# Optimization experiments

Measured on AMD Instinct MI355X. Metric: run time of the kernel, lower is better.

Reference implementation:

```python
import jax, jax.numpy as jnp
import numpy as np

B, S, D, H = 32, 512, 512, 1024  # batch, seq, latents_dims, hidden (=prod(out_dims))


def setup_inputs() -> dict:
    key = jax.random.key(0)
    ks = jax.random.split(key, 7)
    scale_ih = 1.0 / np.sqrt(D)
    scale_hh = 1.0 / np.sqrt(H)
    return {
        "x": jax.random.normal(ks[0], (B, S, D), dtype=jnp.float32),
        "h0": jax.random.uniform(ks[1], (B, H), dtype=jnp.float32),
        "c0": jax.random.uniform(ks[2], (B, H), dtype=jnp.float32),
        "W_ih": jax.random.normal(ks[3], (4 * H, D), dtype=jnp.float32) * scale_ih,
        "W_hh": jax.random.normal(ks[4], (4 * H, H), dtype=jnp.float32) * scale_hh,
        "b_ih": jax.random.normal(ks[5], (4 * H,), dtype=jnp.float32) * scale_hh,
        "b_hh": jax.random.normal(ks[6], (4 * H,), dtype=jnp.float32) * scale_hh,
    }


def reference(x, h0, c0, W_ih, W_hh, b_ih, b_hh):
    # Single-layer LSTM, PyTorch gate order (i, f, g, o).
    # Precompute the input projection for all timesteps in one GEMM: [B,S,4H]
    x_proj = jnp.einsum("bsd,gd->bsg", x, W_ih) + b_ih + b_hh
    xs = jnp.swapaxes(x_proj, 0, 1)  # [S, B, 4H]

    def step(carry, xp_t):
        h, c = carry  # [B, H] each
        gates = xp_t + h @ W_hh.T  # [B, 4H]
        i, f, g, o = jnp.split(gates, 4, axis=-1)
        i = jax.nn.sigmoid(i)
        f = jax.nn.sigmoid(f)
        g = jnp.tanh(g)
        o = jax.nn.sigmoid(o)
        c = f * c + i * g
        h = o * jnp.tanh(c)
        return (h, c), h

    _, hs = jax.lax.scan(step, (h0, c0), xs)  # hs: [S, B, H]
    out = jnp.swapaxes(hs, 0, 1)  # [B, S, H]
    # view(*x.shape[:2], *out_dims) with out_dims=[1024] is a no-op reshape
    return out.reshape(B, S, H)
```

## Files before the change

kernel.cpp:

```cpp
#include <hip/hip_runtime.h>

typedef __bf16 bf16_t;
typedef __bf16 bf16x8 __attribute__((ext_vector_type(8)));
typedef __bf16 bf16x4 __attribute__((ext_vector_type(4)));
typedef __bf16 bf16x2 __attribute__((ext_vector_type(2)));
typedef float f32x16 __attribute__((ext_vector_type(16)));
typedef int i32x4 __attribute__((ext_vector_type(4)));

#define SZ_XBF    (16384ull*512*2)
#define SZ_WIH    (4096ull*512*2)
#define SZ_WHH    (4096ull*1024*2)
#define SZ_XPROJ  (16384ull*4096*2)
#define SZ_HTR    (513ull*32*1024*2)
#define OFF_XBF   (0ull)
#define OFF_WIH   (OFF_XBF + SZ_XBF)
#define OFF_WHH   (OFF_WIH + SZ_WIH)
#define OFF_XPROJ (OFF_WHH + SZ_WHH)
#define OFF_HTR   (OFF_XPROJ + SZ_XPROJ)


__global__ __launch_bounds__(256) void convert_pack(
    const float* __restrict__ x, const float* __restrict__ h0,
    const float* __restrict__ Wih, const float* __restrict__ Whh,
    bf16_t* __restrict__ xbf, bf16_t* __restrict__ wihbf,
    bf16_t* __restrict__ whhbf, bf16_t* __restrict__ htr)
{
  long long v = (long long)blockIdx.x * 256 + threadIdx.x;
  if (v < 2097152LL) {
    long long fi = v * 4;
    int b = (int)(fi >> 18);
    int rem = (int)(fi & 0x3FFFF);
    int s = rem >> 9, d = rem & 511;
    float4 f = *(const float4*)(x + fi);
    bf16x4 o; o.x = (bf16_t)f.x; o.y = (bf16_t)f.y; o.z = (bf16_t)f.z; o.w = (bf16_t)f.w;
    *(bf16x4*)(xbf + ((long long)(s*32 + b)*512 + d)) = o;
  } else if (v < 2621440LL) {
    long long fi = (v - 2097152LL) * 4;
    float4 f = *(const float4*)(Wih + fi);
    bf16x4 o; o.x = (bf16_t)f.x; o.y = (bf16_t)f.y; o.z = (bf16_t)f.z; o.w = (bf16_t)f.w;
    *(bf16x4*)(wihbf + fi) = o;
  } else if (v < 3670016LL) {
    long long fi = (v - 2621440LL) * 4;
    float4 f = *(const float4*)(Whh + fi);
    bf16x4 o; o.x = (bf16_t)f.x; o.y = (bf16_t)f.y; o.z = (bf16_t)f.z; o.w = (bf16_t)f.w;
    *(bf16x4*)(whhbf + fi) = o;
  } else if (v < 3678208LL) {
    long long fi = (v - 3670016LL) * 4;
    int b = (int)(fi >> 10), c = (int)(fi & 1023);
    float4 f = *(const float4*)(h0 + fi);
    bf16x4 o; o.x = (bf16_t)f.x; o.y = (bf16_t)f.y; o.z = (bf16_t)f.z; o.w = (bf16_t)f.w;
    *(bf16x4*)(htr + (long long)(c >> 4) * 512 + b * 16 + (c & 15)) = o;
  } else if (v < 5775360LL) {
    long long idx = v - 3678208LL;
    *(int4*)(htr + 32768LL + idx * 8) = make_int4(-1, -1, -1, -1);
  }
}

__global__ __launch_bounds__(256) void xproj_gemm(
    const bf16_t* __restrict__ Xb, const bf16_t* __restrict__ Wb,
    const float* __restrict__ bih, const float* __restrict__ bhh,
    bf16_t* __restrict__ XP)
{
  __shared__ bf16_t As[128*64];
  __shared__ bf16_t Bs[128*64];
  const int tid = threadIdx.x;
  const int lane = tid & 63, wave = tid >> 6;
  const int mhalf = wave & 1, nhalf = wave >> 1;
  const int l31 = lane & 31, khi = lane >> 5;
  const int m0 = blockIdx.x * 128, n0 = blockIdx.y * 128;

  f32x16 acc[2][2] = {};

  for (int kb = 0; kb < 8; ++kb) {
    const int k0 = kb * 64;
    __syncthreads();
#pragma unroll
    for (int j = 0; j < 4; ++j) {
      int cid = j * 256 + tid;
      int r = cid >> 3, bs = cid & 7;
      int bb = bs ^ (r & 7);
      *(bf16x8*)(As + cid * 8) = *(const bf16x8*)(Xb + (long long)(m0 + r) * 512 + k0 + bb * 8);
      *(bf16x8*)(Bs + cid * 8) = *(const bf16x8*)(Wb + (long long)(n0 + r) * 512 + k0 + bb * 8);
    }
    __syncthreads();
#pragma unroll
    for (int ks = 0; ks < 4; ++ks) {
      int blk = ks * 2 + khi;
      bf16x8 af[2], bfr[2];
#pragma unroll
      for (int mt = 0; mt < 2; ++mt) {
        int r = mhalf * 64 + mt * 32 + l31;
        af[mt] = *(const bf16x8*)(As + (r * 8 + (blk ^ (r & 7))) * 8);
      }
#pragma unroll
      for (int nt = 0; nt < 2; ++nt) {
        int r = nhalf * 64 + nt * 32 + l31;
        bfr[nt] = *(const bf16x8*)(Bs + (r * 8 + (blk ^ (r & 7))) * 8);
      }
#pragma unroll
      for (int mt = 0; mt < 2; ++mt)
#pragma unroll
        for (int nt = 0; nt < 2; ++nt)
          acc[mt][nt] = __builtin_amdgcn_mfma_f32_32x32x16_bf16(af[mt], bfr[nt], acc[mt][nt], 0, 0, 0);
    }
  }
#pragma unroll
  for (int nt = 0; nt < 2; ++nt) {
    int ng = n0 + nhalf * 64 + nt * 32 + l31;
    float bias = bih[ng] + bhh[ng];
#pragma unroll
    for (int mt = 0; mt < 2; ++mt) {
#pragma unroll
      for (int r = 0; r < 16; ++r) {
        int row = (r & 3) + 8 * (r >> 2) + 4 * khi;
        long long mg = m0 + mhalf * 64 + mt * 32 + row;
        XP[mg * 4096 + ng] = (bf16_t)(acc[mt][nt][r] + bias);
      }
    }
  }
}

__device__ __forceinline__ float sigf(float x) { return 1.0f / (1.0f + __expf(-x)); }
__device__ __forceinline__ float tanhfast(float x) {
  float e = __expf(-2.0f * fabsf(x));
  float t = (1.0f - e) / (1.0f + e);
  return copysignf(t, x);
}
__device__ __forceinline__ unsigned umax2(unsigned a, unsigned b) { return a > b ? a : b; }
__device__ __forceinline__ unsigned umax4(i32x4 v) {
  return umax2(umax2((unsigned)v[0], (unsigned)v[1]),
               umax2((unsigned)v[2], (unsigned)v[3]));
}

#define LD16(dst, ptr, OFF) \
  asm volatile("global_load_dwordx4 %0, %1, off offset:" OFF " sc0 sc1" \
               : "=v"(dst) : "v"(ptr) : "memory")

__global__ __launch_bounds__(256, 1) void lstm_rec(
    const bf16_t* __restrict__ Whh_b, const bf16_t* __restrict__ XP,
    const float* __restrict__ c0, float* __restrict__ OUT,
    bf16_t* __restrict__ HTR)
{
  const int tid = threadIdx.x;
  const int lane = tid & 63, wave = tid >> 6;
  const int ntile = wave & 1, khalf = wave >> 1;
  const int wg = blockIdx.x;
  const int l31 = lane & 31, khi = lane >> 5;

  const int nl = ntile * 32 + l31;
  const int grow = (nl >> 4) * 1024 + wg * 16 + (nl & 15);
  const int kbase = khalf * 512 + khi * 8;
  bf16x8 wreg[32];
#pragma unroll
  for (int s = 0; s < 32; ++s)
    wreg[s] = *(const bf16x8*)(Whh_b + (long long)grow * 1024 + kbase + s * 16);

  const char* abase = (const char*)HTR + khalf * 32768 + l31 * 32 + khi * 16;

  __shared__ float gLb[2][2][32][65];
  const int m_e = tid >> 3;
  const int jp = (tid & 7) * 2;
  float cr0 = c0[m_e * 1024 + wg * 16 + jp];
  float cr1 = c0[m_e * 1024 + wg * 16 + jp + 1];

  float xp[4][2];
  {
    const bf16_t* xpb = XP + (long long)m_e * 4096 + wg * 16 + jp;
#pragma unroll
    for (int g = 0; g < 4; ++g) {
      bf16x2 v = *(const bf16x2*)(xpb + g * 1024);
      xp[g][0] = (float)v.x; xp[g][1] = (float)v.y;
    }
  }

  float po0 = 0.0f, po1 = 0.0f;

  for (int t = 0; t < 512; ++t) {
    const char* p0 = abase + ((long long)t << 16);
    const char* p1 = p0 + 4096;  const char* p2 = p0 + 8192;
    const char* p3 = p0 + 12288; const char* p4 = p0 + 16384;
    const char* p5 = p0 + 20480; const char* p6 = p0 + 24576;
    const char* p7 = p0 + 28672;
    i32x4 a[32];
    for (;;) {
      LD16(a[0],  p0, "0"); LD16(a[1],  p0, "1024"); LD16(a[2],  p0, "2048"); LD16(a[3],  p0, "3072");
      LD16(a[4],  p1, "0"); LD16(a[5],  p1, "1024"); LD16(a[6],  p1, "2048"); LD16(a[7],  p1, "3072");
      LD16(a[8],  p2, "0"); LD16(a[9],  p2, "1024"); LD16(a[10], p2, "2048"); LD16(a[11], p2, "3072");
      LD16(a[12], p3, "0"); LD16(a[13], p3, "1024"); LD16(a[14], p3, "2048"); LD16(a[15], p3, "3072");
      LD16(a[16], p4, "0"); LD16(a[17], p4, "1024"); LD16(a[18], p4, "2048"); LD16(a[19], p4, "3072");
      LD16(a[20], p5, "0"); LD16(a[21], p5, "1024"); LD16(a[22], p5, "2048"); LD16(a[23], p5, "3072");
      LD16(a[24], p6, "0"); LD16(a[25], p6, "1024"); LD16(a[26], p6, "2048"); LD16(a[27], p6, "3072");
      LD16(a[28], p7, "0"); LD16(a[29], p7, "1024"); LD16(a[30], p7, "2048"); LD16(a[31], p7, "3072");
      asm volatile("s_waitcnt vmcnt(0)" ::: "memory");
      __builtin_amdgcn_sched_barrier(0);
      unsigned mA = 0, mB = 0, mC = 0, mD = 0;
#pragma unroll
      for (int s = 0; s < 32; s += 4) {
        mA = umax2(mA, umax4(a[s]));
        mB = umax2(mB, umax4(a[s + 1]));
        mC = umax2(mC, umax4(a[s + 2]));
        mD = umax2(mD, umax4(a[s + 3]));
      }
      unsigned mx = umax2(umax2(mA, mB), umax2(mC, mD));
      if (!__any((int)(mx == 0xFFFFFFFFu))) break;
    }

    if (t > 0)
      *(float2*)(OUT + ((long long)m_e * 512 + (t - 1)) * 1024 + wg * 16 + jp) =
          make_float2(po0, po1);

    f32x16 acc0 = {}, acc1 = {};
#pragma unroll
    for (int s = 0; s < 16; ++s)
      acc0 = __builtin_amdgcn_mfma_f32_32x32x16_bf16(
          __builtin_bit_cast(bf16x8, a[s]), wreg[s], acc0, 0, 0, 0);
#pragma unroll
    for (int s = 16; s < 32; ++s)
      acc1 = __builtin_amdgcn_mfma_f32_32x32x16_bf16(
          __builtin_bit_cast(bf16x8, a[s]), wreg[s], acc1, 0, 0, 0);

    float (*gp)[32][65] = gLb[t & 1];
#pragma unroll
    for (int r = 0; r < 16; ++r) {
      int mm = (r & 3) + 8 * (r >> 2) + 4 * khi;
      gp[khalf][mm][nl] = acc0[r] + acc1[r];
    }
    __syncthreads();

    float hv[2];
    {
      float ir  = gp[0][m_e][jp]      + gp[1][m_e][jp]      + xp[0][0];
      float fr  = gp[0][m_e][16 + jp] + gp[1][m_e][16 + jp] + xp[1][0];
      float gr  = gp[0][m_e][32 + jp] + gp[1][m_e][32 + jp] + xp[2][0];
      float orr = gp[0][m_e][48 + jp] + gp[1][m_e][48 + jp] + xp[3][0];
      float c = sigf(fr) * cr0 + sigf(ir) * tanhfast(gr);
      cr0 = c;
      hv[0] = sigf(orr) * tanhfast(c);
    }
    {
      int j = jp + 1;
      float ir  = gp[0][m_e][j]      + gp[1][m_e][j]      + xp[0][1];
      float fr  = gp[0][m_e][16 + j] + gp[1][m_e][16 + j] + xp[1][1];
      float gr  = gp[0][m_e][32 + j] + gp[1][m_e][32 + j] + xp[2][1];
      float orr = gp[0][m_e][48 + j] + gp[1][m_e][48 + j] + xp[3][1];
      float c = sigf(fr) * cr1 + sigf(ir) * tanhfast(gr);
      cr1 = c;
      hv[1] = sigf(orr) * tanhfast(c);
    }

    {
      bf16x2 h2; h2.x = (bf16_t)hv[0]; h2.y = (bf16_t)hv[1];
      unsigned int u = __builtin_bit_cast(unsigned int, h2);
      unsigned int* dst = (unsigned int*)(HTR + (long long)(t + 1) * 32768 +
                                          (long long)wg * 512 + m_e * 16 + jp);
      __hip_atomic_store(dst, u, __ATOMIC_RELAXED, __HIP_MEMORY_SCOPE_AGENT);
    }
    po0 = hv[0]; po1 = hv[1];

    if (t < 511) {
      const bf16_t* xpb = XP + ((long long)(t + 1) * 32 + m_e) * 4096 + wg * 16 + jp;
#pragma unroll
      for (int g = 0; g < 4; ++g) {
        bf16x2 v = *(const bf16x2*)(xpb + g * 1024);
        xp[g][0] = (float)v.x; xp[g][1] = (float)v.y;
      }
    }
  }
  *(float2*)(OUT + ((long long)m_e * 512 + 511) * 1024 + wg * 16 + jp) =
      make_float2(po0, po1);
}

extern "C" void kernel_launch(void* const* d_in, const int* in_sizes, int n_in,
                              void* d_out, int out_size, void* d_ws, size_t ws_size,
                              hipStream_t stream)
{
  const float* x   = (const float*)d_in[0];
  const float* h0  = (const float*)d_in[1];
  const float* c0  = (const float*)d_in[2];
  const float* Wih = (const float*)d_in[3];
  const float* Whh = (const float*)d_in[4];
  const float* bih = (const float*)d_in[5];
  const float* bhh = (const float*)d_in[6];
  float* out = (float*)d_out;

  char* ws = (char*)d_ws;
  bf16_t* xbf   = (bf16_t*)(ws + OFF_XBF);
  bf16_t* wihbf = (bf16_t*)(ws + OFF_WIH);
  bf16_t* whhbf = (bf16_t*)(ws + OFF_WHH);
  bf16_t* xproj = (bf16_t*)(ws + OFF_XPROJ);
  bf16_t* htr   = (bf16_t*)(ws + OFF_HTR);

  convert_pack<<<22560, 256, 0, stream>>>(x, h0, Wih, Whh, xbf, wihbf, whhbf, htr);
  xproj_gemm<<<dim3(128, 32), 256, 0, stream>>>(xbf, wihbf, bih, bhh, xproj);
  lstm_rec<<<64, 256, 0, stream>>>(whhbf, xproj, c0, out, htr);
}
```

Baseline: 1.786 ms.

## Split recurrent GEMM K across four waves, each covering both N tiles

Each of the four waves now owns a quarter of the K dimension and computes both 32-column gate tiles, instead of splitting into two N tiles times two K halves. Each wave loads half as much h data per step (16 instead of 32 vectors) and reuses each A fragment for two MFMAs. The spin-wait poll covers less data, which may shorten the critical path. The cost is a larger shared buffer and four partial sums to add in the gate epilogue instead of two.

```diff
diff --git a/kernel.cpp b/kernel.cpp
--- a/kernel.cpp
+++ b/kernel.cpp
@@ -143,21 +143,23 @@
 {
   const int tid = threadIdx.x;
   const int lane = tid & 63, wave = tid >> 6;
-  const int ntile = wave & 1, khalf = wave >> 1;
+  const int kq = wave;
   const int wg = blockIdx.x;
   const int l31 = lane & 31, khi = lane >> 5;
 
-  const int nl = ntile * 32 + l31;
-  const int grow = (nl >> 4) * 1024 + wg * 16 + (nl & 15);
-  const int kbase = khalf * 512 + khi * 8;
-  bf16x8 wreg[32];
-#pragma unroll
-  for (int s = 0; s < 32; ++s)
-    wreg[s] = *(const bf16x8*)(Whh_b + (long long)grow * 1024 + kbase + s * 16);
-
-  const char* abase = (const char*)HTR + khalf * 32768 + l31 * 32 + khi * 16;
-
-  __shared__ float gLb[2][2][32][65];
+  const int g0row = (l31 >> 4) * 1024 + wg * 16 + (l31 & 15);
+  const int g1row = (2 + (l31 >> 4)) * 1024 + wg * 16 + (l31 & 15);
+  const int kqb = kq * 256 + khi * 8;
+  bf16x8 w0[16], w1[16];
+#pragma unroll
+  for (int s = 0; s < 16; ++s) {
+    w0[s] = *(const bf16x8*)(Whh_b + (long long)g0row * 1024 + kqb + s * 16);
+    w1[s] = *(const bf16x8*)(Whh_b + (long long)g1row * 1024 + kqb + s * 16);
+  }
+
+  const char* abase = (const char*)HTR + kq * 16384 + l31 * 32 + khi * 16;
+
+  __shared__ float gLb[2][4][32][65];
   const int m_e = tid >> 3;
   const int jp = (tid & 7) * 2;
   float cr0 = c0[m_e * 1024 + wg * 16 + jp];
@@ -177,25 +179,20 @@
 
   for (int t = 0; t < 512; ++t) {
     const char* p0 = abase + ((long long)t << 16);
-    const char* p1 = p0 + 4096;  const char* p2 = p0 + 8192;
-    const char* p3 = p0 + 12288; const char* p4 = p0 + 16384;
-    const char* p5 = p0 + 20480; const char* p6 = p0 + 24576;
-    const char* p7 = p0 + 28672;
-    i32x4 a[32];
+    const char* p1 = p0 + 4096;
+    const char* p2 = p0 + 8192;
+    const char* p3 = p0 + 12288;
+    i32x4 a[16];
     for (;;) {
       LD16(a[0],  p0, "0"); LD16(a[1],  p0, "1024"); LD16(a[2],  p0, "2048"); LD16(a[3],  p0, "3072");
       LD16(a[4],  p1, "0"); LD16(a[5],  p1, "1024"); LD16(a[6],  p1, "2048"); LD16(a[7],  p1, "3072");
       LD16(a[8],  p2, "0"); LD16(a[9],  p2, "1024"); LD16(a[10], p2, "2048"); LD16(a[11], p2, "3072");
       LD16(a[12], p3, "0"); LD16(a[13], p3, "1024"); LD16(a[14], p3, "2048"); LD16(a[15], p3, "3072");
-      LD16(a[16], p4, "0"); LD16(a[17], p4, "1024"); LD16(a[18], p4, "2048"); LD16(a[19], p4, "3072");
-      LD16(a[20], p5, "0"); LD16(a[21], p5, "1024"); LD16(a[22], p5, "2048"); LD16(a[23], p5, "3072");
-      LD16(a[24], p6, "0"); LD16(a[25], p6, "1024"); LD16(a[26], p6, "2048"); LD16(a[27], p6, "3072");
-      LD16(a[28], p7, "0"); LD16(a[29], p7, "1024"); LD16(a[30], p7, "2048"); LD16(a[31], p7, "3072");
       asm volatile("s_waitcnt vmcnt(0)" ::: "memory");
       __builtin_amdgcn_sched_barrier(0);
       unsigned mA = 0, mB = 0, mC = 0, mD = 0;
 #pragma unroll
-      for (int s = 0; s < 32; s += 4) {
+      for (int s = 0; s < 16; s += 4) {
         mA = umax2(mA, umax4(a[s]));
         mB = umax2(mB, umax4(a[s + 1]));
         mC = umax2(mC, umax4(a[s + 2]));
@@ -211,38 +208,38 @@
 
     f32x16 acc0 = {}, acc1 = {};
 #pragma unroll
-    for (int s = 0; s < 16; ++s)
-      acc0 = __builtin_amdgcn_mfma_f32_32x32x16_bf16(
-          __builtin_bit_cast(bf16x8, a[s]), wreg[s], acc0, 0, 0, 0);
-#pragma unroll
-    for (int s = 16; s < 32; ++s)
-      acc1 = __builtin_amdgcn_mfma_f32_32x32x16_bf16(
-          __builtin_bit_cast(bf16x8, a[s]), wreg[s], acc1, 0, 0, 0);
-
-    float (*gp)[32][65] = gLb[t & 1];
+    for (int s = 0; s < 16; ++s) {
+      bf16x8 af = __builtin_bit_cast(bf16x8, a[s]);
+      acc0 = __builtin_amdgcn_mfma_f32_32x32x16_bf16(af, w0[s], acc0, 0, 0, 0);
+      acc1 = __builtin_amdgcn_mfma_f32_32x32x16_bf16(af, w1[s], acc1, 0, 0, 0);
+    }
+
+    float (*gp)[65] = gLb[t & 1][kq];
 #pragma unroll
     for (int r = 0; r < 16; ++r) {
       int mm = (r & 3) + 8 * (r >> 2) + 4 * khi;
-      gp[khalf][mm][nl] = acc0[r] + acc1[r];
+      gp[mm][l31]      = acc0[r];
+      gp[mm][32 + l31] = acc1[r];
     }
     __syncthreads();
 
+    float (*ge)[32][65] = gLb[t & 1];
     float hv[2];
     {
-      float ir  = gp[0][m_e][jp]      + gp[1][m_e][jp]      + xp[0][0];
-      float fr  = gp[0][m_e][16 + jp] + gp[1][m_e][16 + jp] + xp[1][0];
-      float gr  = gp[0][m_e][32 + jp] + gp[1][m_e][32 + jp] + xp[2][0];
-      float orr = gp[0][m_e][48 + jp] + gp[1][m_e][48 + jp] + xp[3][0];
+      float ir  = ge[0][m_e][jp]      + ge[1][m_e][jp]      + ge[2][m_e][jp]      + ge[3][m_e][jp]      + xp[0][0];
+      float fr  = ge[0][m_e][16 + jp] + ge[1][m_e][16 + jp] + ge[2][m_e][16 + jp] + ge[3][m_e][16 + jp] + xp[1][0];
+      float gr  = ge[0][m_e][32 + jp] + ge[1][m_e][32 + jp] + ge[2][m_e][32 + jp] + ge[3][m_e][32 + jp] + xp[2][0];
+      float orr = ge[0][m_e][48 + jp] + ge[1][m_e][48 + jp] + ge[2][m_e][48 + jp] + ge[3][m_e][48 + jp] + xp[3][0];
       float c = sigf(fr) * cr0 + sigf(ir) * tanhfast(gr);
       cr0 = c;
       hv[0] = sigf(orr) * tanhfast(c);
     }
     {
       int j = jp + 1;
-      float ir  = gp[0][m_e][j]      + gp[1][m_e][j]      + xp[0][1];
-      float fr  = gp[0][m_e][16 + j] + gp[1][m_e][16 + j] + xp[1][1];
-      float gr  = gp[0][m_e][32 + j] + gp[1][m_e][32 + j] + xp[2][1];
-      float orr = gp[0][m_e][48 + j] + gp[1][m_e][48 + j] + xp[3][1];
+      float ir  = ge[0][m_e][j]      + ge[1][m_e][j]      + ge[2][m_e][j]      + ge[3][m_e][j]      + xp[0][1];
+      float fr  = ge[0][m_e][16 + j] + ge[1][m_e][16 + j] + ge[2][m_e][16 + j] + ge[3][m_e][16 + j] + xp[1][1];
+      float gr  = ge[0][m_e][32 + j] + ge[1][m_e][32 + j] + ge[2][m_e][32 + j] + ge[3][m_e][32 + j] + xp[2][1];
+      float orr = ge[0][m_e][48 + j] + ge[1][m_e][48 + j] + ge[2][m_e][48 + j] + ge[3][m_e][48 + j] + xp[3][1];
       float c = sigf(fr) * cr1 + sigf(ir) * tanhfast(gr);
       cr1 = c;
       hv[1] = sigf(orr) * tanhfast(c);
```

After: 1.530 ms. 14.3% less time.
